# Kernel optimization log

Measured on AMD Instinct MI355X. Metric: run time of the kernel, lower is better.

## Reference

```python
import jax, jax.numpy as jnp
import numpy as np

N_NODES = 100_000
N_EDGES = 1_600_000
D_IN = 128
D_HID = 64   # hard-coded hidden width in Embedder.__init__
D_OUT = 128  # embed_dim
N_GRAPHS = 512


def setup_inputs() -> dict:
    key = jax.random.key(0)
    ks = jax.random.split(key, 10)
    x = jax.random.normal(ks[0], (N_NODES, D_IN), dtype=jnp.float32)
    edge_index = jax.random.randint(ks[1], (2, N_EDGES), 0, N_NODES, dtype=jnp.int64)
    batch_index = jnp.sort(jax.random.randint(ks[2], (N_NODES,), 0, N_GRAPHS, dtype=jnp.int64))
    def glorot(k, fan_in, fan_out):
        s = 1.0 / np.sqrt(fan_in)
        return jax.random.uniform(k, (fan_in, fan_out), jnp.float32, -s, s)
    # layer 1: SAGEConv(D_IN -> D_HID); layer 2: SAGEConv(D_HID -> D_OUT)
    return {
        "x": x,
        "W1_l": glorot(ks[3], D_IN, D_HID),   # applied to mean-aggregated neighbors
        "W1_r": glorot(ks[4], D_IN, D_HID),   # applied to root node
        "b1": jnp.zeros((D_HID,), jnp.float32),
        "W2_l": glorot(ks[5], D_HID, D_OUT),
        "W2_r": glorot(ks[6], D_HID, D_OUT),
        "b2": jnp.zeros((D_OUT,), jnp.float32),
        "edge_index": edge_index,
        "batch_index": batch_index,
    }


def _sage_conv(x, edge_index, W_l, W_r, b):
    # PyG SAGEConv with mean aggregation:
    # out_i = (mean_{j in N(i)} x_j) @ W_l + x_i @ W_r + b
    src, dst = edge_index[0], edge_index[1]
    n = x.shape[0]
    agg = jax.ops.segment_sum(x[src], dst, num_segments=n)          # [N, F]
    deg = jax.ops.segment_sum(jnp.ones((src.shape[0],), x.dtype), dst, num_segments=n)
    mean_nbr = agg / jnp.maximum(deg, 1.0)[:, None]
    return mean_nbr @ W_l + x @ W_r + b


def reference(x, W1_l, W1_r, b1, W2_l, W2_r, b2, edge_index, batch_index):
    h = _sage_conv(x, edge_index, W1_l, W1_r, b1)
    h = jax.nn.relu(h)
    h = _sage_conv(h, edge_index, W2_l, W2_r, b2)
    # F.dropout(p=0.5, training=False) -> identity in eval mode
    # gap: global mean pool per graph
    sums = jax.ops.segment_sum(h, batch_index, num_segments=N_GRAPHS)
    cnts = jax.ops.segment_sum(jnp.ones((h.shape[0],), h.dtype), batch_index, num_segments=N_GRAPHS)
    return sums / jnp.maximum(cnts, 1.0)[:, None]
```

## Files before the change

kernel.cpp:

```cpp
#include <hip/hip_runtime.h>

#define NN   100000
#define NE   1600000
#define DIN  128
#define DH   64
#define DOUT 128
#define NG   512

#define NB   391
#define EPB  6250
#define MSZ  (NB*256)

typedef short short8 __attribute__((ext_vector_type(8)));
typedef float floatx4 __attribute__((ext_vector_type(4)));

__device__ __forceinline__ unsigned short f2bf(float f) {
  unsigned b = __float_as_uint(f);
  b += 0x7FFF + ((b >> 16) & 1);
  return (unsigned short)(b >> 16);
}
__device__ __forceinline__ float bflo(unsigned u) {
  return __uint_as_float(u << 16);
}
__device__ __forceinline__ float bfhi(unsigned u) {
  return __uint_as_float(u & 0xFFFF0000u);
}
__device__ __forceinline__ unsigned pack2(float a, float b) {
  return (unsigned)f2bf(a) | ((unsigned)f2bf(b) << 16);
}

__global__ __launch_bounds__(256) void histA_kernel(
    const int* __restrict__ dst, int* __restrict__ cnt) {
  __shared__ int h[NB];
  for (int i = threadIdx.x; i < NB; i += 256) h[i] = 0;
  __syncthreads();
  int start = blockIdx.x * EPB, end = start + EPB;
  for (int e = start + threadIdx.x; e < end; e += 256)
    atomicAdd(&h[dst[e] >> 8], 1);
  __syncthreads();
  for (int b = threadIdx.x; b < NB; b += 256)
    cnt[b * 256 + blockIdx.x] = h[b];
}

__global__ __launch_bounds__(256) void reduce_kernel(
    const int* __restrict__ cnt, int* __restrict__ partials) {
  __shared__ int s[256];
  int i = blockIdx.x * 256 + threadIdx.x;
  s[threadIdx.x] = cnt[i];
  __syncthreads();
  for (int off = 128; off > 0; off >>= 1) {
    if (threadIdx.x < off) s[threadIdx.x] += s[threadIdx.x + off];
    __syncthreads();
  }
  if (threadIdx.x == 0) partials[blockIdx.x] = s[0];
}

__global__ __launch_bounds__(256) void scanpart_kernel(int* __restrict__ partials) {
  __shared__ int s[NB];
  for (int i = threadIdx.x; i < NB; i += 256) s[i] = partials[i];
  __syncthreads();
  if (threadIdx.x == 0) {
    int run = 0;
    for (int i = 0; i < NB; ++i) { int v = s[i]; s[i] = run; run += v; }
  }
  __syncthreads();
  for (int i = threadIdx.x; i < NB; i += 256) partials[i] = s[i];
}

__global__ __launch_bounds__(256) void scanfinal_kernel(
    const int* __restrict__ cnt, const int* __restrict__ partials,
    int* __restrict__ scanned) {
  __shared__ int s[256];
  int t = threadIdx.x;
  int i = blockIdx.x * 256 + t;
  int c = cnt[i];
  s[t] = c;
  __syncthreads();
  for (int off = 1; off < 256; off <<= 1) {
    int v = (t >= off) ? s[t - off] : 0;
    __syncthreads();
    s[t] += v;
    __syncthreads();
  }
  scanned[i] = s[t] - c + partials[blockIdx.x];
}

__global__ __launch_bounds__(256) void partA_kernel(
    const int* __restrict__ src, const int* __restrict__ dst,
    const int* __restrict__ scanned, int* __restrict__ part) {
  __shared__ int cur[NB];
  for (int i = threadIdx.x; i < NB; i += 256)
    cur[i] = scanned[i * 256 + blockIdx.x];
  __syncthreads();
  int start = blockIdx.x * EPB, end = start + EPB;
  for (int e = start + threadIdx.x; e < end; e += 256) {
    int d = dst[e], s = src[e];
    int pos = atomicAdd(&cur[d >> 8], 1);
    part[pos] = ((d & 255) << 17) | s;
  }
}

__global__ __launch_bounds__(256) void bucket_csr_kernel(
    const int* __restrict__ part, const int* __restrict__ scanned,
    int* __restrict__ row_start, int* __restrict__ eidx) {
  int b = blockIdx.x, t = threadIdx.x;
  int ebeg = scanned[b * 256];
  int eend = (b == NB - 1) ? NE : scanned[(b + 1) * 256];
  int nbase = b << 8;
  int nloc = NN - nbase; if (nloc > 256) nloc = 256;
  __shared__ int cntL[256];
  __shared__ int exclL[256];
  cntL[t] = 0;
  __syncthreads();
  for (int e = ebeg + t; e < eend; e += 256)
    atomicAdd(&cntL[part[e] >> 17], 1);
  __syncthreads();
  int c = cntL[t];
  exclL[t] = c;
  __syncthreads();
  for (int off = 1; off < 256; off <<= 1) {
    int v = (t >= off) ? exclL[t - off] : 0;
    __syncthreads();
    exclL[t] += v;
    __syncthreads();
  }
  int excl = exclL[t] - c;
  if (t < nloc) row_start[nbase + t] = ebeg + excl;
  if (b == NB - 1 && t == 0) row_start[NN] = NE;
  cntL[t] = excl;
  __syncthreads();
  for (int e = ebeg + t; e < eend; e += 256) {
    int v = part[e];
    int pos = atomicAdd(&cntL[v >> 17], 1);
    eidx[ebeg + pos] = v & 0x1FFFF;
  }
}

__global__ __launch_bounds__(256) void bounds_kernel(
    const int* __restrict__ batch, int* __restrict__ gs) {
  int g = blockIdx.x * 256 + threadIdx.x;
  if (g > NG) return;
  if (g == NG) { gs[NG] = NN; return; }
  int lo = 0, hi = NN;
  while (lo < hi) {
    int mid = (lo + hi) >> 1;
    if (batch[mid] < g) lo = mid + 1; else hi = mid;
  }
  gs[g] = lo;
}

__global__ __launch_bounds__(256) void split_w_kernel(
    const float* __restrict__ W1l, const float* __restrict__ W1r,
    short* __restrict__ wfrag) {
  int i = blockIdx.x * 256 + threadIdx.x;
  if (i >= DIN * DH) return;
  int k = i >> 6, n = i & 63;
  int kt = k >> 5, kin = k & 31;
  int lane = ((kin >> 3) << 4) | (n & 15);
  int j8 = kin & 7;
  int jt = n >> 4;
  float wl = W1l[i], wr = W1r[i];
  unsigned bl_ = __float_as_uint(wl);
  unsigned br_ = __float_as_uint(wr);
  short hl = (short)(bl_ >> 16);
  short hr = (short)(br_ >> 16);
  float rl = wl - __uint_as_float(bl_ & 0xFFFF0000u);
  float rr = wr - __uint_as_float(br_ & 0xFFFF0000u);
  short ll = (short)(__float_as_uint(rl) >> 16);
  short lr = (short)(__float_as_uint(rr) >> 16);
  int base0 = (((kt * 2 + 0) * 4 + jt) * 2) * 512 + lane * 8 + j8;
  int base1 = (((kt * 2 + 1) * 4 + jt) * 2) * 512 + lane * 8 + j8;
  wfrag[base0]       = hl;
  wfrag[base0 + 512] = ll;
  wfrag[base1]       = hr;
  wfrag[base1 + 512] = lr;
}

__global__ __launch_bounds__(256) void proj_mfma_kernel(
    const float* __restrict__ x, const short* __restrict__ wfrag,
    const float* __restrict__ b1, unsigned short* __restrict__ xlb,
    unsigned short* __restrict__ xrb) {
  __shared__ short sB[32768];
  {
    const float4* wf4 = (const float4*)wfrag;
    float4* sB4 = (float4*)sB;
    for (int i = threadIdx.x; i < 4096; i += 256) sB4[i] = wf4[i];
  }
  __syncthreads();

  int wave = threadIdx.x >> 6;
  int lane = threadIdx.x & 63;
  int m = lane & 15, q = lane >> 4;
  int tpair = blockIdx.x * 4 + wave;
  int tile0 = tpair * 2, tile1 = tile0 + 1;
  if (tile0 >= 6250) return;

  int r0 = tile0 * 16 + m;
  int r1 = tile1 * 16 + m; if (r1 > NN - 1) r1 = NN - 1;
  const float4* xa = (const float4*)x + (size_t)r0 * 32 + q * 2;
  const float4* xb = (const float4*)x + (size_t)r1 * 32 + q * 2;

  floatx4 acc0[8], acc1[8];
#pragma unroll
  for (int a = 0; a < 8; ++a) {
    acc0[a] = (floatx4){0.f, 0.f, 0.f, 0.f};
    acc1[a] = (floatx4){0.f, 0.f, 0.f, 0.f};
  }

#pragma unroll
  for (int kt = 0; kt < 4; ++kt) {
    float4 p0 = xa[kt * 8];
    float4 p1 = xa[kt * 8 + 1];
    float4 p2 = xb[kt * 8];
    float4 p3 = xb[kt * 8 + 1];
    float af0[8] = {p0.x, p0.y, p0.z, p0.w, p1.x, p1.y, p1.z, p1.w};
    float af1[8] = {p2.x, p2.y, p2.z, p2.w, p3.x, p3.y, p3.z, p3.w};
    short8 ah0, al0, ah1, al1;
#pragma unroll
    for (int e = 0; e < 8; ++e) {
      unsigned b0 = __float_as_uint(af0[e]);
      ah0[e] = (short)(b0 >> 16);
      float lo0 = af0[e] - __uint_as_float(b0 & 0xFFFF0000u);
      al0[e] = (short)(__float_as_uint(lo0) >> 16);
      unsigned b1_ = __float_as_uint(af1[e]);
      ah1[e] = (short)(b1_ >> 16);
      float lo1 = af1[e] - __uint_as_float(b1_ & 0xFFFF0000u);
      al1[e] = (short)(__float_as_uint(lo1) >> 16);
    }
#pragma unroll
    for (int mat = 0; mat < 2; ++mat) {
#pragma unroll
      for (int jt = 0; jt < 4; ++jt) {
        int unit = ((kt * 2 + mat) * 4 + jt) * 2;
        short8 bh = *(const short8*)(sB + unit * 512 + lane * 8);
        short8 bl = *(const short8*)(sB + (unit + 1) * 512 + lane * 8);
        floatx4 c0 = acc0[mat * 4 + jt];
        c0 = __builtin_amdgcn_mfma_f32_16x16x32_bf16(ah0, bh, c0, 0, 0, 0);
        c0 = __builtin_amdgcn_mfma_f32_16x16x32_bf16(ah0, bl, c0, 0, 0, 0);
        c0 = __builtin_amdgcn_mfma_f32_16x16x32_bf16(al0, bh, c0, 0, 0, 0);
        acc0[mat * 4 + jt] = c0;
        floatx4 c1 = acc1[mat * 4 + jt];
        c1 = __builtin_amdgcn_mfma_f32_16x16x32_bf16(ah1, bh, c1, 0, 0, 0);
        c1 = __builtin_amdgcn_mfma_f32_16x16x32_bf16(ah1, bl, c1, 0, 0, 0);
        c1 = __builtin_amdgcn_mfma_f32_16x16x32_bf16(al1, bh, c1, 0, 0, 0);
        acc1[mat * 4 + jt] = c1;
      }
    }
  }

#pragma unroll
  for (int jt = 0; jt < 4; ++jt) {
    int j = jt * 16 + m;
    float bj = b1[j];
    floatx4 cl0 = acc0[jt], cr0 = acc0[4 + jt];
    floatx4 cl1 = acc1[jt], cr1 = acc1[4 + jt];
#pragma unroll
    for (int r = 0; r < 4; ++r) {
      int n0 = tile0 * 16 + q * 4 + r;
      xlb[(size_t)n0 * DH + j] = f2bf(cl0[r]);
      xrb[(size_t)n0 * DH + j] = f2bf(cr0[r] + bj);
    }
    if (tile1 < 6250) {
#pragma unroll
      for (int r = 0; r < 4; ++r) {
        int n1 = tile1 * 16 + q * 4 + r;
        xlb[(size_t)n1 * DH + j] = f2bf(cl1[r]);
        xrb[(size_t)n1 * DH + j] = f2bf(cr1[r] + bj);
      }
    }
  }
}

template <bool RELU_ADD>
__global__ __launch_bounds__(256) void gather_kernel(
    const uint4* __restrict__ feat4, const int* __restrict__ row_start,
    const int* __restrict__ eidx, const uint4* __restrict__ xr4,
    uint4* __restrict__ out4) {
  int t = blockIdx.x * 256 + threadIdx.x;
  int node = t >> 3;
  if (node >= NN) return;
  int fl = t & 7;
  int rs = row_start[node], re = row_start[node + 1];
  float a0 = 0.f, a1 = 0.f, a2 = 0.f, a3 = 0.f;
  float a4 = 0.f, a5 = 0.f, a6 = 0.f, a7 = 0.f;
  int k = rs;
  for (; k + 8 <= re; k += 8) {
    uint4 v[8];
#pragma unroll
    for (int u = 0; u < 8; ++u) v[u] = feat4[(size_t)eidx[k + u] * 8 + fl];
#pragma unroll
    for (int u = 0; u < 8; ++u) {
      a0 += bflo(v[u].x); a1 += bfhi(v[u].x);
      a2 += bflo(v[u].y); a3 += bfhi(v[u].y);
      a4 += bflo(v[u].z); a5 += bfhi(v[u].z);
      a6 += bflo(v[u].w); a7 += bfhi(v[u].w);
    }
  }
  for (; k + 2 <= re; k += 2) {
    uint4 v0 = feat4[(size_t)eidx[k] * 8 + fl];
    uint4 v1 = feat4[(size_t)eidx[k + 1] * 8 + fl];
    a0 += bflo(v0.x) + bflo(v1.x); a1 += bfhi(v0.x) + bfhi(v1.x);
    a2 += bflo(v0.y) + bflo(v1.y); a3 += bfhi(v0.y) + bfhi(v1.y);
    a4 += bflo(v0.z) + bflo(v1.z); a5 += bfhi(v0.z) + bfhi(v1.z);
    a6 += bflo(v0.w) + bflo(v1.w); a7 += bfhi(v0.w) + bfhi(v1.w);
  }
  if (k < re) {
    uint4 v = feat4[(size_t)eidx[k] * 8 + fl];
    a0 += bflo(v.x); a1 += bfhi(v.x);
    a2 += bflo(v.y); a3 += bfhi(v.y);
    a4 += bflo(v.z); a5 += bfhi(v.z);
    a6 += bflo(v.w); a7 += bfhi(v.w);
  }
  float inv = 1.0f / fmaxf((float)(re - rs), 1.0f);
  a0 *= inv; a1 *= inv; a2 *= inv; a3 *= inv;
  a4 *= inv; a5 *= inv; a6 *= inv; a7 *= inv;
  if (RELU_ADD) {
    uint4 r = xr4[(size_t)node * 8 + fl];
    a0 = fmaxf(a0 + bflo(r.x), 0.f); a1 = fmaxf(a1 + bfhi(r.x), 0.f);
    a2 = fmaxf(a2 + bflo(r.y), 0.f); a3 = fmaxf(a3 + bfhi(r.y), 0.f);
    a4 = fmaxf(a4 + bflo(r.z), 0.f); a5 = fmaxf(a5 + bfhi(r.z), 0.f);
    a6 = fmaxf(a6 + bflo(r.w), 0.f); a7 = fmaxf(a7 + bfhi(r.w), 0.f);
  }
  uint4 o;
  o.x = pack2(a0, a1);
  o.y = pack2(a2, a3);
  o.z = pack2(a4, a5);
  o.w = pack2(a6, a7);
  out4[(size_t)node * 8 + fl] = o;
}

__global__ __launch_bounds__(256) void pool_final_kernel(
    const unsigned* __restrict__ hb2, const unsigned* __restrict__ mb2,
    const int* __restrict__ gs, const float* __restrict__ W2l,
    const float* __restrict__ W2r, const float* __restrict__ b2,
    float* __restrict__ out) {
  int g = blockIdx.x;
  int start = gs[g], end = gs[g + 1];
  int slot = threadIdx.x >> 5;
  int j2   = threadIdx.x & 31;
  float sh0 = 0.f, sh1 = 0.f, sm0 = 0.f, sm1 = 0.f;
  for (int n = start + slot; n < end; n += 8) {
    unsigned hv = hb2[(size_t)n * 32 + j2];
    unsigned mv = mb2[(size_t)n * 32 + j2];
    sh0 += bflo(hv); sh1 += bfhi(hv);
    sm0 += bflo(mv); sm1 += bfhi(mv);
  }
  __shared__ float redh[8][DH];
  __shared__ float redm[8][DH];
  redh[slot][j2 * 2] = sh0; redh[slot][j2 * 2 + 1] = sh1;
  redm[slot][j2 * 2] = sm0; redm[slot][j2 * 2 + 1] = sm1;
  __syncthreads();
  __shared__ float hsL[DH], msL[DH];
  if (threadIdx.x < DH) {
    float a = 0.f, b = 0.f;
#pragma unroll
    for (int s = 0; s < 8; ++s) { a += redh[s][threadIdx.x]; b += redm[s][threadIdx.x]; }
    hsL[threadIdx.x] = a; msL[threadIdx.x] = b;
  }
  __syncthreads();
  int j = threadIdx.x;
  if (j < DOUT) {
    float n = (float)(end - start);
    float acc = 0.f;
#pragma unroll 8
    for (int k = 0; k < DH; ++k)
      acc += msL[k] * W2l[k * DOUT + j] + hsL[k] * W2r[k * DOUT + j];
    out[g * DOUT + j] = (acc + n * b2[j]) / fmaxf(n, 1.0f);
  }
}

extern "C" void kernel_launch(void* const* d_in, const int* in_sizes, int n_in,
                              void* d_out, int out_size, void* d_ws, size_t ws_size,
                              hipStream_t stream) {
  (void)in_sizes; (void)n_in; (void)out_size; (void)ws_size;
  const float* x   = (const float*)d_in[0];
  const float* W1l = (const float*)d_in[1];
  const float* W1r = (const float*)d_in[2];
  const float* b1  = (const float*)d_in[3];
  const float* W2l = (const float*)d_in[4];
  const float* W2r = (const float*)d_in[5];
  const float* b2  = (const float*)d_in[6];
  const int*   ei  = (const int*)d_in[7];
  const int*   batch = (const int*)d_in[8];
  const int* src = ei;
  const int* dst = ei + NE;
  float* out = (float*)d_out;

  char* ws = (char*)d_ws;
  unsigned short* xlb = (unsigned short*)(ws);
  unsigned short* hb  = (unsigned short*)(ws + 12800000);
  unsigned short* mb  = (unsigned short*)(ws + 25600000);
  unsigned short* xrb = (unsigned short*)(ws + 38400000);
  int*  part      = (int*)(ws + 51200000);
  int*  cnt       = (int*)(ws + 57600000);
  int*  scanned   = (int*)(ws + 58000384);
  int*  eidx      = (int*)(ws + 76800000);
  int*  row_start = (int*)(ws + 83200000);
  int*   gs       = (int*)(ws + 83600128);
  short* wfrag    = (short*)(ws + 83900032);
  int*  partials  = (int*)(ws + 84400128);

  const int gBlocks = (NN * 8 + 255) / 256;
  const int pBlocks = 782;

  split_w_kernel<<<32, 256, 0, stream>>>(W1l, W1r, wfrag);
  histA_kernel<<<256, 256, 0, stream>>>(dst, cnt);
  reduce_kernel<<<NB, 256, 0, stream>>>(cnt, partials);
  scanpart_kernel<<<1, 256, 0, stream>>>(partials);
  scanfinal_kernel<<<NB, 256, 0, stream>>>(cnt, partials, scanned);
  partA_kernel<<<256, 256, 0, stream>>>(src, dst, scanned, part);
  bucket_csr_kernel<<<NB, 256, 0, stream>>>(part, scanned, row_start, eidx);
  bounds_kernel<<<3, 256, 0, stream>>>(batch, gs);

  proj_mfma_kernel<<<pBlocks, 256, 0, stream>>>(x, wfrag, b1, xlb, xrb);
  gather_kernel<true><<<gBlocks, 256, 0, stream>>>(
      (const uint4*)xlb, row_start, eidx, (const uint4*)xrb, (uint4*)hb);

  gather_kernel<false><<<gBlocks, 256, 0, stream>>>(
      (const uint4*)hb, row_start, eidx, nullptr, (uint4*)mb);

  pool_final_kernel<<<NG, 256, 0, stream>>>(
      (const unsigned*)hb, (const unsigned*)mb, gs, W2l, W2r, b2, out);
}
```

Baseline: 252.8 us.

## Merge independent prep kernels and co-schedule partitioning with projection

Merges the histogram, weight-split and graph-bounds kernels into one launch, using block-index ranges to pick the work. The edge-partition pass and the MFMA projection now share a single launch, with the first 256 blocks partitioning and the rest projecting, so the two independent phases can overlap on the GPU. This cuts launch count and idle tail gaps between small kernels. In exchange, partition blocks reuse the 64KB shared buffer, which may reduce occupancy for those blocks, and mixing two different workloads in one grid can make scheduling uneven.

```diff
diff --git a/kernel.cpp b/kernel.cpp
--- a/kernel.cpp
+++ b/kernel.cpp
@@ -29,17 +29,56 @@
   return (unsigned)f2bf(a) | ((unsigned)f2bf(b) << 16);
 }
 
-__global__ __launch_bounds__(256) void histA_kernel(
-    const int* __restrict__ dst, int* __restrict__ cnt) {
+__global__ __launch_bounds__(256) void prep_kernel(
+    const int* __restrict__ dst, int* __restrict__ cnt,
+    const float* __restrict__ W1l, const float* __restrict__ W1r,
+    short* __restrict__ wfrag, const int* __restrict__ batch,
+    int* __restrict__ gs) {
   __shared__ int h[NB];
-  for (int i = threadIdx.x; i < NB; i += 256) h[i] = 0;
-  __syncthreads();
-  int start = blockIdx.x * EPB, end = start + EPB;
-  for (int e = start + threadIdx.x; e < end; e += 256)
-    atomicAdd(&h[dst[e] >> 8], 1);
-  __syncthreads();
-  for (int b = threadIdx.x; b < NB; b += 256)
-    cnt[b * 256 + blockIdx.x] = h[b];
+  int b = blockIdx.x;
+  if (b < 256) {
+    for (int i = threadIdx.x; i < NB; i += 256) h[i] = 0;
+    __syncthreads();
+    int start = b * EPB, end = start + EPB;
+    for (int e = start + threadIdx.x; e < end; e += 256)
+      atomicAdd(&h[dst[e] >> 8], 1);
+    __syncthreads();
+    for (int bb = threadIdx.x; bb < NB; bb += 256)
+      cnt[bb * 256 + b] = h[bb];
+  } else if (b == 256) {
+    for (int i = threadIdx.x; i < DIN * DH; i += 256) {
+      int k = i >> 6, n = i & 63;
+      int kt = k >> 5, kin = k & 31;
+      int lane = ((kin >> 3) << 4) | (n & 15);
+      int j8 = kin & 7;
+      int jt = n >> 4;
+      float wl = W1l[i], wr = W1r[i];
+      unsigned bl_ = __float_as_uint(wl);
+      unsigned br_ = __float_as_uint(wr);
+      short hl = (short)(bl_ >> 16);
+      short hr = (short)(br_ >> 16);
+      float rl = wl - __uint_as_float(bl_ & 0xFFFF0000u);
+      float rr = wr - __uint_as_float(br_ & 0xFFFF0000u);
+      short ll = (short)(__float_as_uint(rl) >> 16);
+      short lr = (short)(__float_as_uint(rr) >> 16);
+      int base0 = (((kt * 2 + 0) * 4 + jt) * 2) * 512 + lane * 8 + j8;
+      int base1 = (((kt * 2 + 1) * 4 + jt) * 2) * 512 + lane * 8 + j8;
+      wfrag[base0]       = hl;
+      wfrag[base0 + 512] = ll;
+      wfrag[base1]       = hr;
+      wfrag[base1 + 512] = lr;
+    }
+  } else {
+    for (int g = threadIdx.x; g <= NG; g += 256) {
+      if (g == NG) { gs[NG] = NN; continue; }
+      int lo = 0, hi = NN;
+      while (lo < hi) {
+        int mid = (lo + hi) >> 1;
+        if (batch[mid] < g) lo = mid + 1; else hi = mid;
+      }
+      gs[g] = lo;
+    }
+  }
 }
 
 __global__ __launch_bounds__(256) void reduce_kernel(
@@ -85,102 +124,26 @@
   scanned[i] = s[t] - c + partials[blockIdx.x];
 }
 
-__global__ __launch_bounds__(256) void partA_kernel(
+__global__ __launch_bounds__(256) void proj_part_kernel(
     const int* __restrict__ src, const int* __restrict__ dst,
-    const int* __restrict__ scanned, int* __restrict__ part) {
-  __shared__ int cur[NB];
-  for (int i = threadIdx.x; i < NB; i += 256)
-    cur[i] = scanned[i * 256 + blockIdx.x];
-  __syncthreads();
-  int start = blockIdx.x * EPB, end = start + EPB;
-  for (int e = start + threadIdx.x; e < end; e += 256) {
-    int d = dst[e], s = src[e];
-    int pos = atomicAdd(&cur[d >> 8], 1);
-    part[pos] = ((d & 255) << 17) | s;
-  }
-}
-
-__global__ __launch_bounds__(256) void bucket_csr_kernel(
-    const int* __restrict__ part, const int* __restrict__ scanned,
-    int* __restrict__ row_start, int* __restrict__ eidx) {
-  int b = blockIdx.x, t = threadIdx.x;
-  int ebeg = scanned[b * 256];
-  int eend = (b == NB - 1) ? NE : scanned[(b + 1) * 256];
-  int nbase = b << 8;
-  int nloc = NN - nbase; if (nloc > 256) nloc = 256;
-  __shared__ int cntL[256];
-  __shared__ int exclL[256];
-  cntL[t] = 0;
-  __syncthreads();
-  for (int e = ebeg + t; e < eend; e += 256)
-    atomicAdd(&cntL[part[e] >> 17], 1);
-  __syncthreads();
-  int c = cntL[t];
-  exclL[t] = c;
-  __syncthreads();
-  for (int off = 1; off < 256; off <<= 1) {
-    int v = (t >= off) ? exclL[t - off] : 0;
-    __syncthreads();
-    exclL[t] += v;
-    __syncthreads();
-  }
-  int excl = exclL[t] - c;
-  if (t < nloc) row_start[nbase + t] = ebeg + excl;
-  if (b == NB - 1 && t == 0) row_start[NN] = NE;
-  cntL[t] = excl;
-  __syncthreads();
-  for (int e = ebeg + t; e < eend; e += 256) {
-    int v = part[e];
-    int pos = atomicAdd(&cntL[v >> 17], 1);
-    eidx[ebeg + pos] = v & 0x1FFFF;
-  }
-}
-
-__global__ __launch_bounds__(256) void bounds_kernel(
-    const int* __restrict__ batch, int* __restrict__ gs) {
-  int g = blockIdx.x * 256 + threadIdx.x;
-  if (g > NG) return;
-  if (g == NG) { gs[NG] = NN; return; }
-  int lo = 0, hi = NN;
-  while (lo < hi) {
-    int mid = (lo + hi) >> 1;
-    if (batch[mid] < g) lo = mid + 1; else hi = mid;
-  }
-  gs[g] = lo;
-}
-
-__global__ __launch_bounds__(256) void split_w_kernel(
-    const float* __restrict__ W1l, const float* __restrict__ W1r,
-    short* __restrict__ wfrag) {
-  int i = blockIdx.x * 256 + threadIdx.x;
-  if (i >= DIN * DH) return;
-  int k = i >> 6, n = i & 63;
-  int kt = k >> 5, kin = k & 31;
-  int lane = ((kin >> 3) << 4) | (n & 15);
-  int j8 = kin & 7;
-  int jt = n >> 4;
-  float wl = W1l[i], wr = W1r[i];
-  unsigned bl_ = __float_as_uint(wl);
-  unsigned br_ = __float_as_uint(wr);
-  short hl = (short)(bl_ >> 16);
-  short hr = (short)(br_ >> 16);
-  float rl = wl - __uint_as_float(bl_ & 0xFFFF0000u);
-  float rr = wr - __uint_as_float(br_ & 0xFFFF0000u);
-  short ll = (short)(__float_as_uint(rl) >> 16);
-  short lr = (short)(__float_as_uint(rr) >> 16);
-  int base0 = (((kt * 2 + 0) * 4 + jt) * 2) * 512 + lane * 8 + j8;
-  int base1 = (((kt * 2 + 1) * 4 + jt) * 2) * 512 + lane * 8 + j8;
-  wfrag[base0]       = hl;
-  wfrag[base0 + 512] = ll;
-  wfrag[base1]       = hr;
-  wfrag[base1 + 512] = lr;
-}
-
-__global__ __launch_bounds__(256) void proj_mfma_kernel(
+    const int* __restrict__ scanned, int* __restrict__ part,
     const float* __restrict__ x, const short* __restrict__ wfrag,
     const float* __restrict__ b1, unsigned short* __restrict__ xlb,
     unsigned short* __restrict__ xrb) {
   __shared__ short sB[32768];
+  if (blockIdx.x < 256) {
+    int* cur = (int*)sB;
+    for (int i = threadIdx.x; i < NB; i += 256)
+      cur[i] = scanned[i * 256 + blockIdx.x];
+    __syncthreads();
+    int start = blockIdx.x * EPB, end = start + EPB;
+    for (int e = start + threadIdx.x; e < end; e += 256) {
+      int d = dst[e], s = src[e];
+      int pos = atomicAdd(&cur[d >> 8], 1);
+      part[pos] = ((d & 255) << 17) | s;
+    }
+    return;
+  }
   {
     const float4* wf4 = (const float4*)wfrag;
     float4* sB4 = (float4*)sB;
@@ -191,7 +154,7 @@
   int wave = threadIdx.x >> 6;
   int lane = threadIdx.x & 63;
   int m = lane & 15, q = lane >> 4;
-  int tpair = blockIdx.x * 4 + wave;
+  int tpair = (blockIdx.x - 256) * 4 + wave;
   int tile0 = tpair * 2, tile1 = tile0 + 1;
   if (tile0 >= 6250) return;
 
@@ -268,6 +231,42 @@
         xrb[(size_t)n1 * DH + j] = f2bf(cr1[r] + bj);
       }
     }
+  }
+}
+
+__global__ __launch_bounds__(256) void bucket_csr_kernel(
+    const int* __restrict__ part, const int* __restrict__ scanned,
+    int* __restrict__ row_start, int* __restrict__ eidx) {
+  int b = blockIdx.x, t = threadIdx.x;
+  int ebeg = scanned[b * 256];
+  int eend = (b == NB - 1) ? NE : scanned[(b + 1) * 256];
+  int nbase = b << 8;
+  int nloc = NN - nbase; if (nloc > 256) nloc = 256;
+  __shared__ int cntL[256];
+  __shared__ int exclL[256];
+  cntL[t] = 0;
+  __syncthreads();
+  for (int e = ebeg + t; e < eend; e += 256)
+    atomicAdd(&cntL[part[e] >> 17], 1);
+  __syncthreads();
+  int c = cntL[t];
+  exclL[t] = c;
+  __syncthreads();
+  for (int off = 1; off < 256; off <<= 1) {
+    int v = (t >= off) ? exclL[t - off] : 0;
+    __syncthreads();
+    exclL[t] += v;
+    __syncthreads();
+  }
+  int excl = exclL[t] - c;
+  if (t < nloc) row_start[nbase + t] = ebeg + excl;
+  if (b == NB - 1 && t == 0) row_start[NN] = NE;
+  cntL[t] = excl;
+  __syncthreads();
+  for (int e = ebeg + t; e < eend; e += 256) {
+    int v = part[e];
+    int pos = atomicAdd(&cntL[v >> 17], 1);
+    eidx[ebeg + pos] = v & 0x1FFFF;
   }
 }
 
@@ -401,18 +400,16 @@
   int*  partials  = (int*)(ws + 84400128);
 
   const int gBlocks = (NN * 8 + 255) / 256;
-  const int pBlocks = 782;
-
-  split_w_kernel<<<32, 256, 0, stream>>>(W1l, W1r, wfrag);
-  histA_kernel<<<256, 256, 0, stream>>>(dst, cnt);
+
+  prep_kernel<<<258, 256, 0, stream>>>(dst, cnt, W1l, W1r, wfrag, batch, gs);
   reduce_kernel<<<NB, 256, 0, stream>>>(cnt, partials);
   scanpart_kernel<<<1, 256, 0, stream>>>(partials);
   scanfinal_kernel<<<NB, 256, 0, stream>>>(cnt, partials, scanned);
-  partA_kernel<<<256, 256, 0, stream>>>(src, dst, scanned, part);
+
+  proj_part_kernel<<<1038, 256, 0, stream>>>(src, dst, scanned, part,
+                                             x, wfrag, b1, xlb, xrb);
   bucket_csr_kernel<<<NB, 256, 0, stream>>>(part, scanned, row_start, eidx);
-  bounds_kernel<<<3, 256, 0, stream>>>(batch, gs);
-
-  proj_mfma_kernel<<<pBlocks, 256, 0, stream>>>(x, wfrag, b1, xlb, xrb);
+
   gather_kernel<true><<<gBlocks, 256, 0, stream>>>(
       (const uint4*)xlb, row_start, eidx, (const uint4*)xrb, (uint4*)hb);
 
```

After: 247.4 us. -2.1%, faster.
